# Performance work log

Measured on AMD Instinct MI355X. Metric: run time of the kernel, lower is better.

## Reference

```python
import jax, jax.numpy as jnp
import numpy as np

N_NODES = 100000
N_EDGES = 1600000
IN_DIM, HID_DIM, OUT_DIM = 128, 64, 64


def setup_inputs() -> dict:
    key = jax.random.key(0)
    ks = jax.random.split(key, 7)
    x = jax.random.normal(ks[0], (N_NODES, IN_DIM), dtype=jnp.float32)
    edge_index = jax.random.randint(ks[1], (2, N_EDGES), 0, N_NODES, dtype=jnp.int64)
    user_idx = jax.random.randint(ks[2], (N_NODES,), 0, N_NODES, dtype=jnp.int64)
    W1 = jax.random.normal(ks[3], (IN_DIM, HID_DIM), dtype=jnp.float32) * (1.0 / np.sqrt(IN_DIM))
    b1 = jax.random.normal(ks[4], (HID_DIM,), dtype=jnp.float32) * 0.02
    W2 = jax.random.normal(ks[5], (HID_DIM, OUT_DIM), dtype=jnp.float32) * (1.0 / np.sqrt(HID_DIM))
    b2 = jax.random.normal(ks[6], (OUT_DIM,), dtype=jnp.float32) * 0.02
    return {"x": x, "edge_index": edge_index, "user_idx": user_idx,
            "W1": W1, "b1": b1, "W2": W2, "b2": b2}


def _gcn_conv(x, edge_index, W, b):
    # PyG GCNConv: linear transform, add self-loops, sym-normalized aggregation.
    N = x.shape[0]
    h = x @ W  # [N, F_out]
    loop = jnp.arange(N, dtype=edge_index.dtype)
    src = jnp.concatenate([edge_index[0], loop])  # [E+N]
    dst = jnp.concatenate([edge_index[1], loop])
    deg = jax.ops.segment_sum(jnp.ones(src.shape[0], dtype=h.dtype), dst, num_segments=N)
    dis = jnp.where(deg > 0, jax.lax.rsqrt(jnp.maximum(deg, 1.0)), 0.0)  # deg^{-1/2}
    norm = dis[src] * dis[dst]  # [E+N]
    msg = h[src] * norm[:, None]  # gather + scale
    out = jax.ops.segment_sum(msg, dst, num_segments=N)  # scatter-add at targets
    return out + b


def _scatter_mean(x, idx, dim_size):
    s = jax.ops.segment_sum(x, idx, num_segments=dim_size)
    cnt = jax.ops.segment_sum(jnp.ones(x.shape[0], dtype=x.dtype), idx, num_segments=dim_size)
    return jnp.where(cnt[:, None] > 0, s / jnp.maximum(cnt[:, None], 1.0), 0.0)


def reference(x, edge_index, user_idx, W1, b1, W2, b2):
    h = _gcn_conv(x, edge_index, W1, b1)
    h = jax.nn.relu(h)
    # dropout is identity in eval mode
    h = _gcn_conv(h, edge_index, W2, b2)
    return _scatter_mean(h, user_idx, h.shape[0])
```

## Files before the change

### kernel.cpp

```cpp
#include <hip/hip_runtime.h>
#include <hip/hip_bf16.h>


#define FEAT 64
#define INDIM 128

#define SCAN_BS 256
#define SCAN_ELEMS 8
#define SCAN_CHUNK (SCAN_BS * SCAN_ELEMS)

#define BIN_SHIFT 9
#define BIN_R 512
#define BIN_TILE 2048
#define BH_TILE 2048

typedef __attribute__((ext_vector_type(8))) short short8;
typedef __attribute__((ext_vector_type(4))) float f32x4;

__device__ __forceinline__ unsigned short f2bf(float f) {
    unsigned u = __float_as_uint(f);
    unsigned r = u + 0x7FFFu + ((u >> 16) & 1u);
    return (unsigned short)(r >> 16);
}
__device__ __forceinline__ float bf2f(unsigned short v) {
    return __uint_as_float(((unsigned)v) << 16);
}


__global__ __launch_bounds__(256) void k_bhist(const int* __restrict__ dst,
                                               int* __restrict__ gbc, int E, int N, int KB) {
    __shared__ int h[256];
    const int tid = threadIdx.x;
    h[tid] = 0;
    __syncthreads();
    const int base = blockIdx.x * BH_TILE;
    #pragma unroll
    for (int t = 0; t < BH_TILE / 256; ++t) {
        int e = base + t * 256 + tid;
        if (e < E) {
            int d = dst[e];
            if ((unsigned)d < (unsigned)N) atomicAdd(&h[d >> BIN_SHIFT], 1);
        }
    }
    __syncthreads();
    if (tid < KB && h[tid]) atomicAdd(&gbc[tid], h[tid]);
}

__global__ __launch_bounds__(256) void k_bscan(const int* __restrict__ gbc,
                                               int* __restrict__ bb,
                                               int* __restrict__ bcur,
                                               int* __restrict__ rpN, int KB) {
    __shared__ int lds[256];
    const int tid = threadIdx.x;
    int v = (tid < KB) ? gbc[tid] : 0;
    lds[tid] = v;
    __syncthreads();
    for (int d = 1; d < 256; d <<= 1) {
        int t = (tid >= d) ? lds[tid - d] : 0;
        __syncthreads();
        lds[tid] += t;
        __syncthreads();
    }
    int excl = lds[tid] - v;
    if (tid < KB) { bb[tid] = excl; bcur[tid] = excl; }
    if (tid == 255) { bb[KB] = lds[255]; *rpN = lds[255]; }
}

__global__ __launch_bounds__(256) void k_binA(const int* __restrict__ src,
                                              const int* __restrict__ dst,
                                              int* __restrict__ bcur,
                                              unsigned* __restrict__ pairs,
                                              int E, int N, int KB) {
    __shared__ unsigned lbuf[BIN_TILE];
    __shared__ unsigned short bkt[BIN_TILE];
    __shared__ int lcnt[256];
    __shared__ int loff[256];
    __shared__ int lbase[256];
    __shared__ int tot;
    const int tid = threadIdx.x;
    const int base = blockIdx.x * BIN_TILE;

    lcnt[tid] = 0;
    __syncthreads();

    int mys[BIN_TILE / 256], myd[BIN_TILE / 256], myb[BIN_TILE / 256];
    #pragma unroll
    for (int t = 0; t < BIN_TILE / 256; ++t) {
        int e = base + t * 256 + tid;
        int s = 0, d = -1;
        if (e < E) { s = src[e]; d = dst[e]; }
        if ((unsigned)d >= (unsigned)N) d = -1;
        if ((unsigned)s >= (unsigned)N) s = 0;
        mys[t] = s; myd[t] = d;
        myb[t] = (d >= 0) ? (d >> BIN_SHIFT) : -1;
        if (myb[t] >= 0) atomicAdd(&lcnt[myb[t]], 1);
    }
    __syncthreads();

    int v = lcnt[tid];
    loff[tid] = v;
    __syncthreads();
    for (int d = 1; d < 256; d <<= 1) {
        int t2 = (tid >= d) ? loff[tid - d] : 0;
        __syncthreads();
        loff[tid] += t2;
        __syncthreads();
    }
    if (tid == 255) tot = loff[255];
    int excl = loff[tid] - v;
    __syncthreads();
    loff[tid] = excl;
    lcnt[tid] = excl;
    if (tid < KB && v > 0) lbase[tid] = atomicAdd(&bcur[tid], v);
    __syncthreads();

    #pragma unroll
    for (int t = 0; t < BIN_TILE / 256; ++t) {
        if (myb[t] >= 0) {
            int pos = atomicAdd(&lcnt[myb[t]], 1);
            lbuf[pos] = ((unsigned)mys[t] << BIN_SHIFT) | (unsigned)(myd[t] & (BIN_R - 1));
            bkt[pos] = (unsigned short)myb[t];
        }
    }
    __syncthreads();

    const int T = tot;
    for (int i = tid; i < T; i += 256) {
        int b = bkt[i];
        pairs[lbase[b] + (i - loff[b])] = lbuf[i];
    }
}

__global__ __launch_bounds__(1024) void k_binB2(const unsigned* __restrict__ pairs,
                                                const int* __restrict__ bb,
                                                int* __restrict__ rp,
                                                int* __restrict__ col,
                                                float* __restrict__ dis, int N) {
    __shared__ int cnt[BIN_R];
    __shared__ int cur[BIN_R];
    __shared__ int ssum[256];
    const int tid = threadIdx.x;
    const int b = blockIdx.x;
    const int n0 = b << BIN_SHIFT;
    const int n1 = min(n0 + BIN_R, N);
    const int nn = n1 - n0;
    const int e0 = bb[b];
    const int e1 = bb[b + 1];

    for (int i = tid; i < nn; i += 1024) cnt[i] = 0;
    __syncthreads();
    for (int i = e0 + tid; i < e1; i += 1024) {
        atomicAdd(&cnt[pairs[i] & (BIN_R - 1)], 1);
    }
    __syncthreads();

    const int i0 = 2 * tid;
    int c0 = 0, c1 = 0;
    if (tid < 256) {
        c0 = (i0     < nn) ? cnt[i0]     : 0;
        c1 = (i0 + 1 < nn) ? cnt[i0 + 1] : 0;
        ssum[tid] = c0 + c1;
    }
    __syncthreads();
    for (int d = 1; d < 256; d <<= 1) {
        int t = 0;
        if (tid < 256 && tid >= d) t = ssum[tid - d];
        __syncthreads();
        if (tid < 256) ssum[tid] += t;
        __syncthreads();
    }
    if (tid < 256) {
        int excl = ssum[tid] - (c0 + c1);
        if (i0 < nn) {
            cur[i0] = e0 + excl;
            rp[n0 + i0] = e0 + excl;
            dis[n0 + i0] = rsqrtf((float)c0 + 1.0f);
        }
        if (i0 + 1 < nn) {
            cur[i0 + 1] = e0 + excl + c0;
            rp[n0 + i0 + 1] = e0 + excl + c0;
            dis[n0 + i0 + 1] = rsqrtf((float)c1 + 1.0f);
        }
    }
    __syncthreads();

    for (int i = e0 + tid; i < e1; i += 1024) {
        unsigned p = pairs[i];
        int pos = atomicAdd(&cur[p & (BIN_R - 1)], 1);
        col[pos] = (int)(p >> BIN_SHIFT);
    }
}


__global__ __launch_bounds__(256) void k_hist(const int* __restrict__ dst,
                                              int* __restrict__ cntE, int E, int N) {
    int e = blockIdx.x * 256 + threadIdx.x;
    if (e < E) {
        int d = dst[e];
        if ((unsigned)d < (unsigned)N) atomicAdd(&cntE[d], 1);
    }
}
__global__ __launch_bounds__(256) void k_dis(const int* __restrict__ cntE,
                                             float* __restrict__ dis, int N) {
    int i = blockIdx.x * 256 + threadIdx.x;
    if (i < N) dis[i] = rsqrtf((float)cntE[i] + 1.0f);
}
__global__ __launch_bounds__(SCAN_BS) void k_scan1(const int* __restrict__ c,
                                                   int* __restrict__ rp,
                                                   int* __restrict__ ptot, int N) {
    __shared__ int lds[SCAN_BS];
    const int base = blockIdx.x * SCAN_CHUNK;
    const int tb = base + threadIdx.x * SCAN_ELEMS;
    int vals[SCAN_ELEMS];
    int s = 0;
    #pragma unroll
    for (int k = 0; k < SCAN_ELEMS; ++k) {
        int idx = tb + k;
        int v = (idx < N) ? c[idx] : 0;
        vals[k] = s;
        s += v;
    }
    lds[threadIdx.x] = s;
    __syncthreads();
    for (int d = 1; d < SCAN_BS; d <<= 1) {
        int v = (threadIdx.x >= d) ? lds[threadIdx.x - d] : 0;
        __syncthreads();
        lds[threadIdx.x] += v;
        __syncthreads();
    }
    int toff = (threadIdx.x == 0) ? 0 : lds[threadIdx.x - 1];
    #pragma unroll
    for (int k = 0; k < SCAN_ELEMS; ++k) {
        int idx = tb + k;
        if (idx < N) rp[idx] = toff + vals[k];
    }
    if (threadIdx.x == SCAN_BS - 1) ptot[blockIdx.x] = lds[SCAN_BS - 1];
}
__global__ __launch_bounds__(1024) void k_scan2(int* __restrict__ ptot,
                                                int* __restrict__ poff,
                                                int* __restrict__ rpN, int nb) {
    __shared__ int lds[1024];
    int tid = threadIdx.x;
    lds[tid] = (tid < nb) ? ptot[tid] : 0;
    __syncthreads();
    for (int d = 1; d < 1024; d <<= 1) {
        int v = (tid >= d) ? lds[tid - d] : 0;
        __syncthreads();
        lds[tid] += v;
        __syncthreads();
    }
    if (tid < nb) poff[tid] = (tid == 0) ? 0 : lds[tid - 1];
    if (tid == nb - 1) *rpN = lds[tid];
}
__global__ __launch_bounds__(SCAN_BS) void k_scan3(int* __restrict__ rp,
                                                   const int* __restrict__ poff, int N) {
    int off = poff[blockIdx.x];
    const int tb = blockIdx.x * SCAN_CHUNK + threadIdx.x * SCAN_ELEMS;
    #pragma unroll
    for (int k = 0; k < SCAN_ELEMS; ++k) {
        int idx = tb + k;
        if (idx < N) rp[idx] += off;
    }
}
__global__ __launch_bounds__(256) void k_fill(const int* __restrict__ src,
                                              const int* __restrict__ dst,
                                              const int* __restrict__ rp,
                                              int* __restrict__ tmp,
                                              int* __restrict__ col, int E, int N) {
    int e = blockIdx.x * 256 + threadIdx.x;
    if (e >= E) return;
    int s = src[e], d = dst[e];
    if ((unsigned)s >= (unsigned)N) s = 0;
    if ((unsigned)d >= (unsigned)N) return;
    int r = atomicAdd(&tmp[d], 1);
    col[rp[d] + r] = s;
}

__global__ __launch_bounds__(256) void k_ucnt(const int* __restrict__ uidx,
                                              float* __restrict__ cntf, int N) {
    int i = blockIdx.x * 256 + threadIdx.x;
    if (i < N) {
        int u = uidx[i];
        if ((unsigned)u < (unsigned)N) atomicAdd(&cntf[u], 1.0f);
    }
}

__global__ __launch_bounds__(256) void k_inv(float* __restrict__ c, int N) {
    int i = blockIdx.x * 256 + threadIdx.x;
    if (i < N) {
        float v = c[i];
        c[i] = (v > 0.f) ? (1.0f / v) : 0.f;
    }
}


__global__ __launch_bounds__(256) void k_gemm1(const float* __restrict__ x,
                                               const float* __restrict__ W,
                                               const float* __restrict__ scale,
                                               unsigned short* __restrict__ out, int N) {
    __shared__ short wf[4 * 4 * 64 * 8];
    const int tid = threadIdx.x;
    for (int i = tid; i < INDIM * FEAT; i += 256) {
        int k = i >> 6, n = i & 63;
        int ct = n >> 4, kc = k >> 5, r = k & 31;
        int owner = ((r >> 3) << 4) | (n & 15);
        wf[(((ct << 2) | kc) * 64 + owner) * 8 + (r & 7)] = (short)f2bf(W[i]);
    }
    __syncthreads();

    const int lane = tid & 63;
    const int m = lane & 15, q = lane >> 4;
    const int row0 = blockIdx.x * 64 + (tid >> 6) * 16;

    short8 bfr[4][4];
    #pragma unroll
    for (int ct = 0; ct < 4; ++ct)
        #pragma unroll
        for (int kc = 0; kc < 4; ++kc)
            bfr[ct][kc] = *reinterpret_cast<const short8*>(&wf[(((ct << 2) | kc) * 64 + lane) * 8]);

    int gr = row0 + m;
    int rl = gr < N ? gr : (N - 1);
    const float* xp = x + (long)rl * INDIM + q * 8;

    f32x4 acc[4] = {{0,0,0,0},{0,0,0,0},{0,0,0,0},{0,0,0,0}};
    #pragma unroll
    for (int kc = 0; kc < 4; ++kc) {
        float4 v0 = *reinterpret_cast<const float4*>(xp + kc * 32);
        float4 v1 = *reinterpret_cast<const float4*>(xp + kc * 32 + 4);
        short8 a;
        a[0]=(short)f2bf(v0.x); a[1]=(short)f2bf(v0.y); a[2]=(short)f2bf(v0.z); a[3]=(short)f2bf(v0.w);
        a[4]=(short)f2bf(v1.x); a[5]=(short)f2bf(v1.y); a[6]=(short)f2bf(v1.z); a[7]=(short)f2bf(v1.w);
        #pragma unroll
        for (int ct = 0; ct < 4; ++ct)
            acc[ct] = __builtin_amdgcn_mfma_f32_16x16x32_bf16(a, bfr[ct][kc], acc[ct], 0, 0, 0);
    }

    #pragma unroll
    for (int reg = 0; reg < 4; ++reg) {
        int row = row0 + q * 4 + reg;
        if (row < N) {
            float sc = scale[row];
            #pragma unroll
            for (int ct = 0; ct < 4; ++ct)
                out[(long)row * FEAT + ct * 16 + m] = f2bf(acc[ct][reg] * sc);
        }
    }
}

__global__ __launch_bounds__(256) void k_gemm2(const unsigned short* __restrict__ h,
                                               const float* __restrict__ W,
                                               const float* __restrict__ scale,
                                               unsigned short* __restrict__ out, int N) {
    __shared__ short wf[4 * 2 * 64 * 8];
    const int tid = threadIdx.x;
    for (int i = tid; i < FEAT * FEAT; i += 256) {
        int k = i >> 6, n = i & 63;
        int ct = n >> 4, kc = k >> 5, r = k & 31;
        int owner = ((r >> 3) << 4) | (n & 15);
        wf[(((ct << 1) | kc) * 64 + owner) * 8 + (r & 7)] = (short)f2bf(W[i]);
    }
    __syncthreads();

    const int lane = tid & 63;
    const int m = lane & 15, q = lane >> 4;
    const int row0 = blockIdx.x * 64 + (tid >> 6) * 16;

    short8 bfr[4][2];
    #pragma unroll
    for (int ct = 0; ct < 4; ++ct)
        #pragma unroll
        for (int kc = 0; kc < 2; ++kc)
            bfr[ct][kc] = *reinterpret_cast<const short8*>(&wf[(((ct << 1) | kc) * 64 + lane) * 8]);

    int gr = row0 + m;
    int rl = gr < N ? gr : (N - 1);
    const unsigned short* hp = h + (long)rl * FEAT + q * 8;

    f32x4 acc[4] = {{0,0,0,0},{0,0,0,0},{0,0,0,0},{0,0,0,0}};
    #pragma unroll
    for (int kc = 0; kc < 2; ++kc) {
        short8 a = *reinterpret_cast<const short8*>(hp + kc * 32);
        #pragma unroll
        for (int ct = 0; ct < 4; ++ct)
            acc[ct] = __builtin_amdgcn_mfma_f32_16x16x32_bf16(a, bfr[ct][kc], acc[ct], 0, 0, 0);
    }

    #pragma unroll
    for (int reg = 0; reg < 4; ++reg) {
        int row = row0 + q * 4 + reg;
        if (row < N) {
            float sc = scale[row];
            #pragma unroll
            for (int ct = 0; ct < 4; ++ct)
                out[(long)row * FEAT + ct * 16 + m] = f2bf(acc[ct][reg] * sc);
        }
    }
}


#define ACC8(r, mm)                                                              \
    a0 = fmaf(mm, bf2f((unsigned short)(r).x),         a0);                      \
    a1 = fmaf(mm, bf2f((unsigned short)((r).x >> 16)), a1);                      \
    a2 = fmaf(mm, bf2f((unsigned short)(r).y),         a2);                      \
    a3 = fmaf(mm, bf2f((unsigned short)((r).y >> 16)), a3);                      \
    a4 = fmaf(mm, bf2f((unsigned short)(r).z),         a4);                      \
    a5 = fmaf(mm, bf2f((unsigned short)((r).z >> 16)), a5);                      \
    a6 = fmaf(mm, bf2f((unsigned short)(r).w),         a6);                      \
    a7 = fmaf(mm, bf2f((unsigned short)((r).w >> 16)), a7);

#define AGG_BODY(SELF_INIT)                                                      \
    const int lane = threadIdx.x & 63;                                           \
    const int q2 = lane >> 3;                                                    \
    const int ol = lane & 7;                                                     \
    const int jb = rp[i], je = rp[i + 1];                                        \
    float a0=0.f,a1=0.f,a2=0.f,a3=0.f,a4=0.f,a5=0.f,a6=0.f,a7=0.f;               \
    if (q2 == 0) { SELF_INIT }                                                   \
    for (int j0 = jb; j0 < je; j0 += 32) {                                       \
        int j1 = j0 + q2, j2 = j0 + 8 + q2, j3 = j0 + 16 + q2, j4 = j0 + 24 + q2;\
        int c1 = (j1 < je) ? col[j1] : i;  float m1 = (j1 < je) ? 1.f : 0.f;     \
        int c2 = (j2 < je) ? col[j2] : i;  float m2 = (j2 < je) ? 1.f : 0.f;     \
        int c3 = (j3 < je) ? col[j3] : i;  float m3 = (j3 < je) ? 1.f : 0.f;     \
        int c4 = (j4 < je) ? col[j4] : i;  float m4 = (j4 < je) ? 1.f : 0.f;     \
        uint4 r1 = *reinterpret_cast<const uint4*>(A + (long)c1 * FEAT + 8 * ol);\
        uint4 r2 = *reinterpret_cast<const uint4*>(A + (long)c2 * FEAT + 8 * ol);\
        uint4 r3 = *reinterpret_cast<const uint4*>(A + (long)c3 * FEAT + 8 * ol);\
        uint4 r4 = *reinterpret_cast<const uint4*>(A + (long)c4 * FEAT + 8 * ol);\
        ACC8(r1, m1)                                                             \
        ACC8(r2, m2)                                                             \
        ACC8(r3, m3)                                                             \
        ACC8(r4, m4)                                                             \
    }                                                                            \
    a0 += __shfl_xor(a0, 8);  a1 += __shfl_xor(a1, 8);                           \
    a2 += __shfl_xor(a2, 8);  a3 += __shfl_xor(a3, 8);                           \
    a4 += __shfl_xor(a4, 8);  a5 += __shfl_xor(a5, 8);                           \
    a6 += __shfl_xor(a6, 8);  a7 += __shfl_xor(a7, 8);                           \
    a0 += __shfl_xor(a0, 16); a1 += __shfl_xor(a1, 16);                          \
    a2 += __shfl_xor(a2, 16); a3 += __shfl_xor(a3, 16);                          \
    a4 += __shfl_xor(a4, 16); a5 += __shfl_xor(a5, 16);                          \
    a6 += __shfl_xor(a6, 16); a7 += __shfl_xor(a7, 16);                          \
    a0 += __shfl_xor(a0, 32); a1 += __shfl_xor(a1, 32);                          \
    a2 += __shfl_xor(a2, 32); a3 += __shfl_xor(a3, 32);                          \
    a4 += __shfl_xor(a4, 32); a5 += __shfl_xor(a5, 32);                          \
    a6 += __shfl_xor(a6, 32); a7 += __shfl_xor(a7, 32);

__global__ __launch_bounds__(256) void k_agg1(const unsigned short* __restrict__ A,
                                              const int* __restrict__ rp,
                                              const int* __restrict__ col,
                                              const float* __restrict__ dis,
                                              const float* __restrict__ bias,
                                              unsigned short* __restrict__ H, int N) {
    int i = blockIdx.x * 4 + (threadIdx.x >> 6);
    if (i >= N) return;
    AGG_BODY(
        uint4 rv = *reinterpret_cast<const uint4*>(A + (long)i * FEAT + 8 * ol);
        a0 = bf2f((unsigned short)rv.x); a1 = bf2f((unsigned short)(rv.x >> 16));
        a2 = bf2f((unsigned short)rv.y); a3 = bf2f((unsigned short)(rv.y >> 16));
        a4 = bf2f((unsigned short)rv.z); a5 = bf2f((unsigned short)(rv.z >> 16));
        a6 = bf2f((unsigned short)rv.w); a7 = bf2f((unsigned short)(rv.w >> 16));
    )
    if (q2 == 0) {
        float di = dis[i];
        float4 b4a = *reinterpret_cast<const float4*>(bias + 8 * ol);
        float4 b4b = *reinterpret_cast<const float4*>(bias + 8 * ol + 4);
        uint4 o;
        o.x = (unsigned)f2bf(fmaxf(fmaf(di, a0, b4a.x), 0.f))
            | ((unsigned)f2bf(fmaxf(fmaf(di, a1, b4a.y), 0.f)) << 16);
        o.y = (unsigned)f2bf(fmaxf(fmaf(di, a2, b4a.z), 0.f))
            | ((unsigned)f2bf(fmaxf(fmaf(di, a3, b4a.w), 0.f)) << 16);
        o.z = (unsigned)f2bf(fmaxf(fmaf(di, a4, b4b.x), 0.f))
            | ((unsigned)f2bf(fmaxf(fmaf(di, a5, b4b.y), 0.f)) << 16);
        o.w = (unsigned)f2bf(fmaxf(fmaf(di, a6, b4b.z), 0.f))
            | ((unsigned)f2bf(fmaxf(fmaf(di, a7, b4b.w), 0.f)) << 16);
        *reinterpret_cast<uint4*>(H + (long)i * FEAT + 8 * ol) = o;
    }
}

__global__ __launch_bounds__(256) void k_agg2s(const unsigned short* __restrict__ A,
                                               const int* __restrict__ rp,
                                               const int* __restrict__ col,
                                               const float* __restrict__ dis,
                                               const float* __restrict__ bias,
                                               const int* __restrict__ uidx,
                                               const float* __restrict__ invc,
                                               float* __restrict__ S, int N) {
    int i = blockIdx.x * 4 + (threadIdx.x >> 6);
    if (i >= N) return;
    AGG_BODY(
        uint4 rv = *reinterpret_cast<const uint4*>(A + (long)i * FEAT + 8 * ol);
        a0 = bf2f((unsigned short)rv.x); a1 = bf2f((unsigned short)(rv.x >> 16));
        a2 = bf2f((unsigned short)rv.y); a3 = bf2f((unsigned short)(rv.y >> 16));
        a4 = bf2f((unsigned short)rv.z); a5 = bf2f((unsigned short)(rv.z >> 16));
        a6 = bf2f((unsigned short)rv.w); a7 = bf2f((unsigned short)(rv.w >> 16));
    )
    int u = uidx[i];
    if ((unsigned)u < (unsigned)N) {
        float di = dis[i];
        float w = invc[u];
        float v = (q2 == 0) ? a0 : (q2 == 1) ? a1 : (q2 == 2) ? a2 : (q2 == 3) ? a3
                : (q2 == 4) ? a4 : (q2 == 5) ? a5 : (q2 == 6) ? a6 : a7;
        int f = 8 * ol + q2;
        atomicAdd(&S[(long)u * FEAT + f], w * fmaf(di, v, bias[f]));
    }
}

extern "C" void kernel_launch(void* const* d_in, const int* in_sizes, int n_in,
                              void* d_out, int out_size, void* d_ws, size_t ws_size,
                              hipStream_t stream) {
    const float* x   = (const float*)d_in[0];
    const int* edge  = (const int*)d_in[1];
    const int* uidx  = (const int*)d_in[2];
    const float* W1  = (const float*)d_in[3];
    const float* b1  = (const float*)d_in[4];
    const float* W2  = (const float*)d_in[5];
    const float* b2  = (const float*)d_in[6];
    float* out       = (float*)d_out;

    const int N = in_sizes[2];
    const int E = in_sizes[1] / 2;
    const int* src = edge;
    const int* dst = edge + E;

    const size_t fbuf = (size_t)N * FEAT * sizeof(float);
    const size_t abuf = (size_t)N * FEAT * sizeof(unsigned short);
    const int gE  = (E + 255) / 256;
    const int gN  = (N + 255) / 256;
    const int gN4 = (N + 3) / 4;
    const int gG  = (N + 63) / 64;
    const int nbScan = (N + SCAN_CHUNK - 1) / SCAN_CHUNK;
    const int KB = (N + BIN_R - 1) >> BIN_SHIFT;

    auto align256 = [](size_t v) { return (v + 255) & ~(size_t)255; };

    char* w = (char*)d_ws;
    size_t o = 0;
    float* dis  = (float*)(w + o); o = align256(o + (size_t)N * 4);
    float* cntf = (float*)(w + o); o = align256(o + (size_t)N * 4);
    int*   rp   = (int*)  (w + o); o = align256(o + (size_t)(N + 1) * 4);
    int*   cntE = (int*)  (w + o); o = align256(o + (size_t)N * 4);
    int*   ptot = (int*)  (w + o); o = align256(o + (size_t)1024 * 4);
    int*   poff = (int*)  (w + o); o = align256(o + (size_t)1024 * 4);
    int*   col  = (int*)  (w + o); o = align256(o + (size_t)E * 4);
    size_t apsz = (size_t)E * 4 > abuf ? (size_t)E * 4 : abuf;
    char*  Ap   = w + o;           o = align256(o + apsz);
    const size_t need = o;
    int* gbc  = cntE;
    int* bb   = ptot;
    int* bcur = poff;
    unsigned* pairs = (unsigned*)Ap;
    unsigned short* A = (unsigned short*)Ap;
    unsigned short* Hb = (unsigned short*)out;

    if (ws_size >= need && KB <= 256 && N <= (1 << (32 - BIN_SHIFT - 1))) {
        hipMemsetAsync(gbc, 0, (size_t)KB * 4, stream);
        k_bhist<<<(E + BH_TILE - 1) / BH_TILE, 256, 0, stream>>>(dst, gbc, E, N, KB);
        k_bscan<<<1, 256, 0, stream>>>(gbc, bb, bcur, rp + N, KB);
        k_binA <<<(E + BIN_TILE - 1) / BIN_TILE, 256, 0, stream>>>(src, dst, bcur, pairs, E, N, KB);
        k_binB2<<<KB, 1024, 0, stream>>>(pairs, bb, rp, col, dis, N);
        hipMemsetAsync(cntf, 0, (size_t)N * 4, stream);
        k_ucnt <<<gN, 256, 0, stream>>>(uidx, cntf, N);
        k_inv  <<<gN, 256, 0, stream>>>(cntf, N);

        k_gemm1<<<gG, 256, 0, stream>>>(x, W1, dis, A, N);
        k_agg1 <<<gN4, 256, 0, stream>>>(A, rp, col, dis, b1, Hb, N);

        k_gemm2<<<gG, 256, 0, stream>>>(Hb, W2, dis, A, N);
        hipMemsetAsync(out, 0, fbuf, stream);
        k_agg2s<<<gN4, 256, 0, stream>>>(A, rp, col, dis, b2, uidx, cntf, out, N);
    } else {
        hipMemsetAsync(cntE, 0, (size_t)N * 4, stream);
        k_hist <<<gE, 256, 0, stream>>>(dst, cntE, E, N);
        k_dis  <<<gN, 256, 0, stream>>>(cntE, dis, N);
        k_scan1<<<nbScan, SCAN_BS, 0, stream>>>(cntE, rp, ptot, N);
        k_scan2<<<1, 1024, 0, stream>>>(ptot, poff, rp + N, nbScan);
        k_scan3<<<nbScan, SCAN_BS, 0, stream>>>(rp, poff, N);
        hipMemsetAsync(cntE, 0, (size_t)N * 4, stream);
        k_fill <<<gE, 256, 0, stream>>>(src, dst, rp, cntE, col, E, N);
        hipMemsetAsync(cntf, 0, (size_t)N * 4, stream);
        k_ucnt <<<gN, 256, 0, stream>>>(uidx, cntf, N);
        k_inv  <<<gN, 256, 0, stream>>>(cntf, N);
        k_gemm1<<<gG, 256, 0, stream>>>(x, W1, dis, A, N);
        k_agg1 <<<gN4, 256, 0, stream>>>(A, rp, col, dis, b1, Hb, N);
        k_gemm2<<<gG, 256, 0, stream>>>(Hb, W2, dis, A, N);
        hipMemsetAsync(out, 0, fbuf, stream);
        k_agg2s<<<gN4, 256, 0, stream>>>(A, rp, col, dis, b2, uidx, cntf, out, N);
    }
}
```

Before: 286.7 us.

## Process four nodes per wavefront in GCN aggregation with zero sentinel row

Restructures the CSR aggregation kernels so each 64-lane wavefront handles four destination nodes (16 lanes each) instead of one. With average degree near 16, the old mapping left most lanes masked. Padded neighbour slots now read an all-zero sentinel row N written by the GEMM kernels, which removes the per-edge mask multiply and turns the FMA into an add. The separate reciprocal-count kernel is folded into agg2s, and cross-lane reductions shrink to one shuffle stage. The tradeoff is more per-lane loop iterations and divergence across nodes of different degree, plus eight atomics per active lane in the final scatter.

```diff
diff --git a/kernel.cpp b/kernel.cpp
--- a/kernel.cpp
+++ b/kernel.cpp
@@ -285,14 +285,6 @@
     }
 }
 
-__global__ __launch_bounds__(256) void k_inv(float* __restrict__ c, int N) {
-    int i = blockIdx.x * 256 + threadIdx.x;
-    if (i < N) {
-        float v = c[i];
-        c[i] = (v > 0.f) ? (1.0f / v) : 0.f;
-    }
-}
-
 
 __global__ __launch_bounds__(256) void k_gemm1(const float* __restrict__ x,
                                                const float* __restrict__ W,
@@ -300,6 +292,10 @@
                                                unsigned short* __restrict__ out, int N) {
     __shared__ short wf[4 * 4 * 64 * 8];
     const int tid = threadIdx.x;
+    if (blockIdx.x == 0 && tid < 8) {
+        uint4 z; z.x = 0; z.y = 0; z.z = 0; z.w = 0;
+        *reinterpret_cast<uint4*>(out + (long)N * FEAT + tid * 8) = z;
+    }
     for (int i = tid; i < INDIM * FEAT; i += 256) {
         int k = i >> 6, n = i & 63;
         int ct = n >> 4, kc = k >> 5, r = k & 31;
@@ -354,6 +350,10 @@
                                                unsigned short* __restrict__ out, int N) {
     __shared__ short wf[4 * 2 * 64 * 8];
     const int tid = threadIdx.x;
+    if (blockIdx.x == 0 && tid < 8) {
+        uint4 z; z.x = 0; z.y = 0; z.z = 0; z.w = 0;
+        *reinterpret_cast<uint4*>(out + (long)N * FEAT + tid * 8) = z;
+    }
     for (int i = tid; i < FEAT * FEAT; i += 256) {
         int k = i >> 6, n = i & 63;
         int ct = n >> 4, kc = k >> 5, r = k & 31;
@@ -399,50 +399,46 @@
 }
 
 
-#define ACC8(r, mm)                                                              \
-    a0 = fmaf(mm, bf2f((unsigned short)(r).x),         a0);                      \
-    a1 = fmaf(mm, bf2f((unsigned short)((r).x >> 16)), a1);                      \
-    a2 = fmaf(mm, bf2f((unsigned short)(r).y),         a2);                      \
-    a3 = fmaf(mm, bf2f((unsigned short)((r).y >> 16)), a3);                      \
-    a4 = fmaf(mm, bf2f((unsigned short)(r).z),         a4);                      \
-    a5 = fmaf(mm, bf2f((unsigned short)((r).z >> 16)), a5);                      \
-    a6 = fmaf(mm, bf2f((unsigned short)(r).w),         a6);                      \
-    a7 = fmaf(mm, bf2f((unsigned short)((r).w >> 16)), a7);
+#define ACC8(r)                                                                  \
+    a0 += bf2f((unsigned short)(r).x);                                           \
+    a1 += bf2f((unsigned short)((r).x >> 16));                                   \
+    a2 += bf2f((unsigned short)(r).y);                                           \
+    a3 += bf2f((unsigned short)((r).y >> 16));                                   \
+    a4 += bf2f((unsigned short)(r).z);                                           \
+    a5 += bf2f((unsigned short)((r).z >> 16));                                   \
+    a6 += bf2f((unsigned short)(r).w);                                           \
+    a7 += bf2f((unsigned short)((r).w >> 16));
 
 #define AGG_BODY(SELF_INIT)                                                      \
     const int lane = threadIdx.x & 63;                                           \
-    const int q2 = lane >> 3;                                                    \
+    const int p  = lane >> 4;                                                    \
+    const int s  = (lane >> 3) & 1;                                              \
     const int ol = lane & 7;                                                     \
-    const int jb = rp[i], je = rp[i + 1];                                        \
+    const int i  = blockIdx.x * 16 + (threadIdx.x >> 6) * 4 + p;                 \
+    const bool valid = (i < N);                                                  \
+    const int jb = valid ? rp[i] : 0;                                            \
+    const int je = valid ? rp[i + 1] : 0;                                        \
     float a0=0.f,a1=0.f,a2=0.f,a3=0.f,a4=0.f,a5=0.f,a6=0.f,a7=0.f;               \
-    if (q2 == 0) { SELF_INIT }                                                   \
-    for (int j0 = jb; j0 < je; j0 += 32) {                                       \
-        int j1 = j0 + q2, j2 = j0 + 8 + q2, j3 = j0 + 16 + q2, j4 = j0 + 24 + q2;\
-        int c1 = (j1 < je) ? col[j1] : i;  float m1 = (j1 < je) ? 1.f : 0.f;     \
-        int c2 = (j2 < je) ? col[j2] : i;  float m2 = (j2 < je) ? 1.f : 0.f;     \
-        int c3 = (j3 < je) ? col[j3] : i;  float m3 = (j3 < je) ? 1.f : 0.f;     \
-        int c4 = (j4 < je) ? col[j4] : i;  float m4 = (j4 < je) ? 1.f : 0.f;     \
+    if (valid && s == 0) { SELF_INIT }                                           \
+    for (int j0 = jb; j0 < je; j0 += 8) {                                        \
+        int j1 = j0 + s, j2 = j1 + 2, j3 = j1 + 4, j4 = j1 + 6;                  \
+        int c1 = (j1 < je) ? col[j1] : N;                                        \
+        int c2 = (j2 < je) ? col[j2] : N;                                        \
+        int c3 = (j3 < je) ? col[j3] : N;                                        \
+        int c4 = (j4 < je) ? col[j4] : N;                                        \
         uint4 r1 = *reinterpret_cast<const uint4*>(A + (long)c1 * FEAT + 8 * ol);\
         uint4 r2 = *reinterpret_cast<const uint4*>(A + (long)c2 * FEAT + 8 * ol);\
         uint4 r3 = *reinterpret_cast<const uint4*>(A + (long)c3 * FEAT + 8 * ol);\
         uint4 r4 = *reinterpret_cast<const uint4*>(A + (long)c4 * FEAT + 8 * ol);\
-        ACC8(r1, m1)                                                             \
-        ACC8(r2, m2)                                                             \
-        ACC8(r3, m3)                                                             \
-        ACC8(r4, m4)                                                             \
+        ACC8(r1)                                                                 \
+        ACC8(r2)                                                                 \
+        ACC8(r3)                                                                 \
+        ACC8(r4)                                                                 \
     }                                                                            \
     a0 += __shfl_xor(a0, 8);  a1 += __shfl_xor(a1, 8);                           \
     a2 += __shfl_xor(a2, 8);  a3 += __shfl_xor(a3, 8);                           \
     a4 += __shfl_xor(a4, 8);  a5 += __shfl_xor(a5, 8);                           \
-    a6 += __shfl_xor(a6, 8);  a7 += __shfl_xor(a7, 8);                           \
-    a0 += __shfl_xor(a0, 16); a1 += __shfl_xor(a1, 16);                          \
-    a2 += __shfl_xor(a2, 16); a3 += __shfl_xor(a3, 16);                          \
-    a4 += __shfl_xor(a4, 16); a5 += __shfl_xor(a5, 16);                          \
-    a6 += __shfl_xor(a6, 16); a7 += __shfl_xor(a7, 16);                          \
-    a0 += __shfl_xor(a0, 32); a1 += __shfl_xor(a1, 32);                          \
-    a2 += __shfl_xor(a2, 32); a3 += __shfl_xor(a3, 32);                          \
-    a4 += __shfl_xor(a4, 32); a5 += __shfl_xor(a5, 32);                          \
-    a6 += __shfl_xor(a6, 32); a7 += __shfl_xor(a7, 32);
+    a6 += __shfl_xor(a6, 8);  a7 += __shfl_xor(a7, 8);
 
 __global__ __launch_bounds__(256) void k_agg1(const unsigned short* __restrict__ A,
                                               const int* __restrict__ rp,
@@ -450,8 +446,6 @@
                                               const float* __restrict__ dis,
                                               const float* __restrict__ bias,
                                               unsigned short* __restrict__ H, int N) {
-    int i = blockIdx.x * 4 + (threadIdx.x >> 6);
-    if (i >= N) return;
     AGG_BODY(
         uint4 rv = *reinterpret_cast<const uint4*>(A + (long)i * FEAT + 8 * ol);
         a0 = bf2f((unsigned short)rv.x); a1 = bf2f((unsigned short)(rv.x >> 16));
@@ -459,7 +453,7 @@
         a4 = bf2f((unsigned short)rv.z); a5 = bf2f((unsigned short)(rv.z >> 16));
         a6 = bf2f((unsigned short)rv.w); a7 = bf2f((unsigned short)(rv.w >> 16));
     )
-    if (q2 == 0) {
+    if (s == 0 && valid) {
         float di = dis[i];
         float4 b4a = *reinterpret_cast<const float4*>(bias + 8 * ol);
         float4 b4b = *reinterpret_cast<const float4*>(bias + 8 * ol + 4);
@@ -482,10 +476,8 @@
                                                const float* __restrict__ dis,
                                                const float* __restrict__ bias,
                                                const int* __restrict__ uidx,
-                                               const float* __restrict__ invc,
+                                               const float* __restrict__ cntf,
                                                float* __restrict__ S, int N) {
-    int i = blockIdx.x * 4 + (threadIdx.x >> 6);
-    if (i >= N) return;
     AGG_BODY(
         uint4 rv = *reinterpret_cast<const uint4*>(A + (long)i * FEAT + 8 * ol);
         a0 = bf2f((unsigned short)rv.x); a1 = bf2f((unsigned short)(rv.x >> 16));
@@ -493,14 +485,24 @@
         a4 = bf2f((unsigned short)rv.z); a5 = bf2f((unsigned short)(rv.z >> 16));
         a6 = bf2f((unsigned short)rv.w); a7 = bf2f((unsigned short)(rv.w >> 16));
     )
-    int u = uidx[i];
-    if ((unsigned)u < (unsigned)N) {
-        float di = dis[i];
-        float w = invc[u];
-        float v = (q2 == 0) ? a0 : (q2 == 1) ? a1 : (q2 == 2) ? a2 : (q2 == 3) ? a3
-                : (q2 == 4) ? a4 : (q2 == 5) ? a5 : (q2 == 6) ? a6 : a7;
-        int f = 8 * ol + q2;
-        atomicAdd(&S[(long)u * FEAT + f], w * fmaf(di, v, bias[f]));
+    if (s == 0 && valid) {
+        int u = uidx[i];
+        if ((unsigned)u < (unsigned)N) {
+            float di = dis[i];
+            float c = cntf[u];
+            float w = (c > 0.f) ? (1.0f / c) : 0.f;
+            float4 b4a = *reinterpret_cast<const float4*>(bias + 8 * ol);
+            float4 b4b = *reinterpret_cast<const float4*>(bias + 8 * ol + 4);
+            float* Sp = S + (long)u * FEAT + 8 * ol;
+            atomicAdd(Sp + 0, w * fmaf(di, a0, b4a.x));
+            atomicAdd(Sp + 1, w * fmaf(di, a1, b4a.y));
+            atomicAdd(Sp + 2, w * fmaf(di, a2, b4a.z));
+            atomicAdd(Sp + 3, w * fmaf(di, a3, b4a.w));
+            atomicAdd(Sp + 4, w * fmaf(di, a4, b4b.x));
+            atomicAdd(Sp + 5, w * fmaf(di, a5, b4b.y));
+            atomicAdd(Sp + 6, w * fmaf(di, a6, b4b.z));
+            atomicAdd(Sp + 7, w * fmaf(di, a7, b4b.w));
+        }
     }
 }
 
@@ -522,11 +524,11 @@
     const int* dst = edge + E;
 
     const size_t fbuf = (size_t)N * FEAT * sizeof(float);
-    const size_t abuf = (size_t)N * FEAT * sizeof(unsigned short);
-    const int gE  = (E + 255) / 256;
-    const int gN  = (N + 255) / 256;
-    const int gN4 = (N + 3) / 4;
-    const int gG  = (N + 63) / 64;
+    const size_t abuf = (size_t)(N + 1) * FEAT * sizeof(unsigned short);
+    const int gE   = (E + 255) / 256;
+    const int gN   = (N + 255) / 256;
+    const int gN16 = (N + 15) / 16;
+    const int gG   = (N + 63) / 64;
     const int nbScan = (N + SCAN_CHUNK - 1) / SCAN_CHUNK;
     const int KB = (N + BIN_R - 1) >> BIN_SHIFT;
 
@@ -559,14 +561,13 @@
         k_binB2<<<KB, 1024, 0, stream>>>(pairs, bb, rp, col, dis, N);
         hipMemsetAsync(cntf, 0, (size_t)N * 4, stream);
         k_ucnt <<<gN, 256, 0, stream>>>(uidx, cntf, N);
-        k_inv  <<<gN, 256, 0, stream>>>(cntf, N);
 
         k_gemm1<<<gG, 256, 0, stream>>>(x, W1, dis, A, N);
-        k_agg1 <<<gN4, 256, 0, stream>>>(A, rp, col, dis, b1, Hb, N);
+        k_agg1 <<<gN16, 256, 0, stream>>>(A, rp, col, dis, b1, Hb, N);
 
         k_gemm2<<<gG, 256, 0, stream>>>(Hb, W2, dis, A, N);
         hipMemsetAsync(out, 0, fbuf, stream);
-        k_agg2s<<<gN4, 256, 0, stream>>>(A, rp, col, dis, b2, uidx, cntf, out, N);
+        k_agg2s<<<gN16, 256, 0, stream>>>(A, rp, col, dis, b2, uidx, cntf, out, N);
     } else {
         hipMemsetAsync(cntE, 0, (size_t)N * 4, stream);
         k_hist <<<gE, 256, 0, stream>>>(dst, cntE, E, N);
@@ -578,11 +579,10 @@
         k_fill <<<gE, 256, 0, stream>>>(src, dst, rp, cntE, col, E, N);
         hipMemsetAsync(cntf, 0, (size_t)N * 4, stream);
         k_ucnt <<<gN, 256, 0, stream>>>(uidx, cntf, N);
-        k_inv  <<<gN, 256, 0, stream>>>(cntf, N);
         k_gemm1<<<gG, 256, 0, stream>>>(x, W1, dis, A, N);
-        k_agg1 <<<gN4, 256, 0, stream>>>(A, rp, col, dis, b1, Hb, N);
+        k_agg1 <<<gN16, 256, 0, stream>>>(A, rp, col, dis, b1, Hb, N);
         k_gemm2<<<gG, 256, 0, stream>>>(Hb, W2, dis, A, N);
         hipMemsetAsync(out, 0, fbuf, stream);
-        k_agg2s<<<gN4, 256, 0, stream>>>(A, rp, col, dis, b2, uidx, cntf, out, N);
-    }
-}
+        k_agg2s<<<gN16, 256, 0, stream>>>(A, rp, col, dis, b2, uidx, cntf, out, N);
+    }
+}
```

Measured after the change: 431.9 us. 1.51x slower.
